# Kernel tuning notes

Measured on AMD Instinct MI355X. Metric: run time of the kernel, lower is better.

The kernel has to match this reference:

```python
import jax, jax.numpy as jnp
import numpy as np

PATCH = 256
CH = 28


def setup_inputs() -> dict:
    key = jax.random.key(0)
    kx, km = jax.random.split(key)
    x = jax.random.normal(kx, (32, PATCH, PATCH, CH), dtype=jnp.float32)
    # bk: binary mask from a (P/2, P/2) random pattern, tiled 2x2, repeated over channels
    ms = PATCH // 2
    bk_fixed = jnp.round(jax.random.uniform(km, (ms, ms), dtype=jnp.float32))
    bk_tile = jnp.tile(bk_fixed, (2, 2))                      # [P, P]
    bk = jnp.repeat(bk_tile[:, :, None], CH, axis=2)          # [P, P, C]
    return {"x": x, "bk": bk}


def reference(x, bk):
    # Original math per channel ch:
    #   y[i,j,ch] = x[(i+ch)%P, j, ch] * bk[i,j,ch]      (roll by -ch, multiply)
    #   z[i,j,ch] = y[(i-ch)%P, j, ch]                   (roll back by +ch)
    # => z[i,j,ch] = x[i,j,ch] * bk[(i-ch)%P, j, ch]
    # So fuse the two rolls into a single per-channel roll of the mask,
    # then a fused multiply + channel-sum (single memory pass).
    C = x.shape[-1]
    shifts = jnp.arange(C)
    # roll each channel of the mask by +ch along height
    bk_shifted = jax.vmap(lambda m, s: jnp.roll(m, s, axis=0),
                          in_axes=(2, 0), out_axes=2)(bk, shifts)  # [P, P, C]
    # fused shift-multiply-accumulate: [B, P, P]
    return jnp.sum(x * bk_shifted[None], axis=-1)
```

## Files before the change

### kernel.cpp

```cpp
#include <hip/hip_runtime.h>

#define P 256
#define C 28
#define NPIX (P * P)
#define MASK_ELEMS (NPIX * C)
#define Q 7
#define BLK 448
#define PIX_PER_BLK 64
#define BLKS_PER_IMG 1024

__global__ __launch_bounds__(256) void prep_mask_kernel(
    const float* __restrict__ bk, float* __restrict__ bks) {
    int idx = blockIdx.x * 256 + threadIdx.x;
    if (idx >= MASK_ELEMS) return;
    int ch = idx % C;
    int ij = idx / C;
    int j = ij & (P - 1);
    int i = ij >> 8;
    int src_row = (i - ch) & (P - 1);
    bks[idx] = bk[(src_row * P + j) * C + ch];
}

__global__ __launch_bounds__(BLK) void codednet_f4_kernel(
    const float4* __restrict__ x4, const float4* __restrict__ m4,
    float* __restrict__ out) {
    __shared__ float s[BLK];
    int t = threadIdx.x;
    int f = blockIdx.x * BLK + t;
    int mf = (blockIdx.x & (BLKS_PER_IMG - 1)) * BLK + t;
    float4 a = x4[f];
    float4 m = m4[mf];
    s[t] = a.x * m.x + a.y * m.y + a.z * m.z + a.w * m.w;
    __syncthreads();
    if (t < PIX_PER_BLK) {
        const float* p = s + t * Q;
        float acc = ((p[0] + p[1]) + (p[2] + p[3])) + ((p[4] + p[5]) + p[6]);
        out[blockIdx.x * PIX_PER_BLK + t] = acc;
    }
}

__global__ __launch_bounds__(256) void codednet_inline_kernel(
    const float* __restrict__ x, const float* __restrict__ bk,
    float* __restrict__ out) {
    int pid = blockIdx.x * 256 + threadIdx.x;
    int pix = pid & (NPIX - 1);
    int j = pix & (P - 1);
    int i = pix >> 8;
    const float* xp = x + (size_t)pid * C;
    float acc = 0.f;
#pragma unroll
    for (int ch = 0; ch < C; ++ch) {
        int src_row = (i - ch) & (P - 1);
        acc += xp[ch] * bk[(src_row * P + j) * C + ch];
    }
    out[pid] = acc;
}

extern "C" void kernel_launch(void* const* d_in, const int* in_sizes, int n_in,
                              void* d_out, int out_size, void* d_ws, size_t ws_size,
                              hipStream_t stream) {
    const float* x  = (const float*)d_in[0];
    const float* bk = (const float*)d_in[1];
    float* out = (float*)d_out;

    const int total = out_size;

    if (ws_size >= (size_t)MASK_ELEMS * sizeof(float)) {
        float* bks = (float*)d_ws;
        prep_mask_kernel<<<(MASK_ELEMS + 255) / 256, 256, 0, stream>>>(bk, bks);
        const int nblocks = total / PIX_PER_BLK;
        codednet_f4_kernel<<<nblocks, BLK, 0, stream>>>(
            (const float4*)x, (const float4*)bks, out);
    } else {
        codednet_inline_kernel<<<(total + 255) / 256, 256, 0, stream>>>(x, bk, out);
    }
}
```

Before: 322.2 us.

## Fuse mask shift into main kernel with XCD-aware block swizzle

Removes the separate mask pre-shift kernel and workspace pass; the main kernel now gathers the rolled mask values directly from bk using per-channel row offsets. Block indices are remapped so each XCD processes a contiguous band of rows across all images, keeping the needed mask rows resident in that XCD's L2. This trades an extra launch and mask write/read for four strided scalar loads per thread.

Measured after the change: 595.6 us. 84.9% more time.

```diff
diff --git a/kernel.cpp b/kernel.cpp
--- a/kernel.cpp
+++ b/kernel.cpp
@@ -3,75 +3,59 @@
 #define P 256
 #define C 28
 #define NPIX (P * P)
-#define MASK_ELEMS (NPIX * C)
+#define NIMG 32
 #define Q 7
 #define BLK 448
 #define PIX_PER_BLK 64
-#define BLKS_PER_IMG 1024
 
-__global__ __launch_bounds__(256) void prep_mask_kernel(
-    const float* __restrict__ bk, float* __restrict__ bks) {
-    int idx = blockIdx.x * 256 + threadIdx.x;
-    if (idx >= MASK_ELEMS) return;
-    int ch = idx % C;
-    int ij = idx / C;
-    int j = ij & (P - 1);
-    int i = ij >> 8;
-    int src_row = (i - ch) & (P - 1);
-    bks[idx] = bk[(src_row * P + j) * C + ch];
-}
-
-__global__ __launch_bounds__(BLK) void codednet_f4_kernel(
-    const float4* __restrict__ x4, const float4* __restrict__ m4,
+__global__ __launch_bounds__(BLK) void codednet_fused_kernel(
+    const float4* __restrict__ x4, const float* __restrict__ bk,
     float* __restrict__ out) {
     __shared__ float s[BLK];
     int t = threadIdx.x;
-    int f = blockIdx.x * BLK + t;
-    int mf = (blockIdx.x & (BLKS_PER_IMG - 1)) * BLK + t;
-    float4 a = x4[f];
-    float4 m = m4[mf];
-    s[t] = a.x * m.x + a.y * m.y + a.z * m.z + a.w * m.w;
+    int n = blockIdx.x;
+
+    int xcd   = n & 7;
+    int g     = n >> 3;
+    int i_loc = g >> 7;
+    int rem   = g & 127;
+    int j0b   = rem & 3;
+    int img   = rem >> 2;
+    int i     = (xcd << 5) + i_loc;
+    int pid0  = (img << 16) + (i << 8) + (j0b << 6);
+
+    int pix_loc = t / 7;
+    int q       = t - pix_loc * 7;
+    int j       = (j0b << 6) + pix_loc;
+    int c0      = q << 2;
+
+    float4 a = x4[pid0 * 7 + t];
+
+    int jc = j * C + c0;
+    int r0 = (i - c0)     & (P - 1);
+    int r1 = (i - c0 - 1) & (P - 1);
+    int r2 = (i - c0 - 2) & (P - 1);
+    int r3 = (i - c0 - 3) & (P - 1);
+    float m0 = bk[r0 * (P * C) + jc];
+    float m1 = bk[r1 * (P * C) + jc + 1];
+    float m2 = bk[r2 * (P * C) + jc + 2];
+    float m3 = bk[r3 * (P * C) + jc + 3];
+
+    s[t] = a.x * m0 + a.y * m1 + a.z * m2 + a.w * m3;
     __syncthreads();
+
     if (t < PIX_PER_BLK) {
         const float* p = s + t * Q;
         float acc = ((p[0] + p[1]) + (p[2] + p[3])) + ((p[4] + p[5]) + p[6]);
-        out[blockIdx.x * PIX_PER_BLK + t] = acc;
+        out[pid0 + t] = acc;
     }
-}
-
-__global__ __launch_bounds__(256) void codednet_inline_kernel(
-    const float* __restrict__ x, const float* __restrict__ bk,
-    float* __restrict__ out) {
-    int pid = blockIdx.x * 256 + threadIdx.x;
-    int pix = pid & (NPIX - 1);
-    int j = pix & (P - 1);
-    int i = pix >> 8;
-    const float* xp = x + (size_t)pid * C;
-    float acc = 0.f;
-#pragma unroll
-    for (int ch = 0; ch < C; ++ch) {
-        int src_row = (i - ch) & (P - 1);
-        acc += xp[ch] * bk[(src_row * P + j) * C + ch];
-    }
-    out[pid] = acc;
 }
 
 extern "C" void kernel_launch(void* const* d_in, const int* in_sizes, int n_in,
                               void* d_out, int out_size, void* d_ws, size_t ws_size,
                               hipStream_t stream) {
-    const float* x  = (const float*)d_in[0];
-    const float* bk = (const float*)d_in[1];
+    const float4* x4 = (const float4*)d_in[0];
+    const float* bk  = (const float*)d_in[1];
     float* out = (float*)d_out;
-
-    const int total = out_size;
-
-    if (ws_size >= (size_t)MASK_ELEMS * sizeof(float)) {
-        float* bks = (float*)d_ws;
-        prep_mask_kernel<<<(MASK_ELEMS + 255) / 256, 256, 0, stream>>>(bk, bks);
-        const int nblocks = total / PIX_PER_BLK;
-        codednet_f4_kernel<<<nblocks, BLK, 0, stream>>>(
-            (const float4*)x, (const float4*)bks, out);
-    } else {
-        codednet_inline_kernel<<<(total + 255) / 256, 256, 0, stream>>>(x, bk, out);
-    }
+    codednet_fused_kernel<<<NIMG * P * (P / PIX_PER_BLK) / 1, BLK, 0, stream>>>(x4, bk, out);
 }
```

## Reuse mask across four images per block with shuffle reduction and XCD-aware mapping

Applied to the files above, without the earlier changes.

Each block now handles a 64-pixel tile for four images. It loads the pre-shifted mask once into registers and reuses it for all four images, which cuts the mask reads. The per-pixel channel sum is done with warp shuffles in groups of 8 lanes instead of through shared memory and a barrier, so one lane in eight sits idle. Block indices are remapped so that consecutive blocks spread over XCDs with contiguous rows per XCD, to improve L2 locality of the mask.

Measured after the change: 328.2 us. About the same (+1.9%).

```diff
diff --git a/kernel.cpp b/kernel.cpp
--- a/kernel.cpp
+++ b/kernel.cpp
@@ -3,11 +3,9 @@
 #define P 256
 #define C 28
 #define NPIX (P * P)
+#define NIMG 32
+#define Q 7
 #define MASK_ELEMS (NPIX * C)
-#define Q 7
-#define BLK 448
-#define PIX_PER_BLK 64
-#define BLKS_PER_IMG 1024
 
 __global__ __launch_bounds__(256) void prep_mask_kernel(
     const float* __restrict__ bk, float* __restrict__ bks) {
@@ -21,21 +19,62 @@
     bks[idx] = bk[(src_row * P + j) * C + ch];
 }
 
-__global__ __launch_bounds__(BLK) void codednet_f4_kernel(
+#define BLK 512
+#define PIX 64
+#define IMG_PER_BLK 4
+#define TILES (P * (P / PIX))
+#define NBLOCKS (TILES * (NIMG / IMG_PER_BLK))
+
+__global__ __launch_bounds__(BLK) void codednet_main_kernel(
     const float4* __restrict__ x4, const float4* __restrict__ m4,
     float* __restrict__ out) {
-    __shared__ float s[BLK];
     int t = threadIdx.x;
-    int f = blockIdx.x * BLK + t;
-    int mf = (blockIdx.x & (BLKS_PER_IMG - 1)) * BLK + t;
-    float4 a = x4[f];
-    float4 m = m4[mf];
-    s[t] = a.x * m.x + a.y * m.y + a.z * m.z + a.w * m.w;
-    __syncthreads();
-    if (t < PIX_PER_BLK) {
-        const float* p = s + t * Q;
-        float acc = ((p[0] + p[1]) + (p[2] + p[3])) + ((p[4] + p[5]) + p[6]);
-        out[blockIdx.x * PIX_PER_BLK + t] = acc;
+    int n = blockIdx.x;
+
+    int g   = n >> 10;
+    int mm  = n & 1023;
+    int xcd   = mm & 7;
+    int loc   = mm >> 3;
+    int i_loc = loc >> 2;
+    int j0b   = loc & 3;
+    int i     = (xcd << 5) + i_loc;
+    int pix0  = (i << 8) + (j0b << 6);
+
+    int q  = t & 7;
+    int pl = t >> 3;
+    int f  = (pix0 + pl) * Q + q;
+
+    float4 mk = make_float4(0.f, 0.f, 0.f, 0.f);
+    if (q < 7) mk = m4[f];
+
+    const size_t istr = (size_t)NPIX * Q;
+    int img0 = g * IMG_PER_BLK;
+
+    float4 a0 = make_float4(0.f,0.f,0.f,0.f), a1 = a0, a2 = a0, a3 = a0;
+    if (q < 7) {
+        const float4* xb = x4 + f;
+        a0 = xb[(size_t)(img0 + 0) * istr];
+        a1 = xb[(size_t)(img0 + 1) * istr];
+        a2 = xb[(size_t)(img0 + 2) * istr];
+        a3 = xb[(size_t)(img0 + 3) * istr];
+    }
+
+    float r0 = a0.x * mk.x + a0.y * mk.y + a0.z * mk.z + a0.w * mk.w;
+    float r1 = a1.x * mk.x + a1.y * mk.y + a1.z * mk.z + a1.w * mk.w;
+    float r2 = a2.x * mk.x + a2.y * mk.y + a2.z * mk.z + a2.w * mk.w;
+    float r3 = a3.x * mk.x + a3.y * mk.y + a3.z * mk.z + a3.w * mk.w;
+
+    r0 += __shfl_xor(r0, 1); r0 += __shfl_xor(r0, 2); r0 += __shfl_xor(r0, 4);
+    r1 += __shfl_xor(r1, 1); r1 += __shfl_xor(r1, 2); r1 += __shfl_xor(r1, 4);
+    r2 += __shfl_xor(r2, 1); r2 += __shfl_xor(r2, 2); r2 += __shfl_xor(r2, 4);
+    r3 += __shfl_xor(r3, 1); r3 += __shfl_xor(r3, 2); r3 += __shfl_xor(r3, 4);
+
+    if (q == 0) {
+        int ob = pix0 + pl;
+        out[(img0 + 0) * NPIX + ob] = r0;
+        out[(img0 + 1) * NPIX + ob] = r1;
+        out[(img0 + 2) * NPIX + ob] = r2;
+        out[(img0 + 3) * NPIX + ob] = r3;
     }
 }
 
@@ -62,14 +101,12 @@
     const float* x  = (const float*)d_in[0];
     const float* bk = (const float*)d_in[1];
     float* out = (float*)d_out;
-
     const int total = out_size;
 
     if (ws_size >= (size_t)MASK_ELEMS * sizeof(float)) {
         float* bks = (float*)d_ws;
         prep_mask_kernel<<<(MASK_ELEMS + 255) / 256, 256, 0, stream>>>(bk, bks);
-        const int nblocks = total / PIX_PER_BLK;
-        codednet_f4_kernel<<<nblocks, BLK, 0, stream>>>(
+        codednet_main_kernel<<<NBLOCKS, BLK, 0, stream>>>(
             (const float4*)x, (const float4*)bks, out);
     } else {
         codednet_inline_kernel<<<(total + 255) / 256, 256, 0, stream>>>(x, bk, out);
```
